# Kernel optimization log

Measured on AMD Instinct MI355X. Metric: run time of the kernel, lower is better.

Reference implementation:

```python
import jax, jax.numpy as jnp
import numpy as np

LN_EPS = 1e-5  # ParlAI LAYER_NORM_EPS
B, S, D, H, E, V = 4, 512, 512, 2048, 8, 32000


def setup_inputs() -> dict:
    key = jax.random.key(0)
    ks = jax.random.split(key, 6)
    x = jax.random.normal(ks[0], (B, S, D), dtype=jnp.float32)
    orig_input = jax.random.randint(ks[1], (B, S), 0, V)          # token ids
    hash_bin_map = jax.random.randint(ks[2], (V,), 0, E, dtype=jnp.int32)
    W1 = jax.random.normal(ks[3], (E, D, H), dtype=jnp.float32) * 0.02
    b1 = jnp.zeros((E, H), dtype=jnp.float32)
    W2 = jax.random.normal(ks[4], (E, H, D), dtype=jnp.float32) * 0.02
    b2 = jnp.zeros((E, D), dtype=jnp.float32)
    gamma = jnp.ones((D,), dtype=jnp.float32)
    beta = jnp.zeros((D,), dtype=jnp.float32)
    return {"x": x, "W1": W1, "b1": b1, "W2": W2, "b2": b2,
            "gamma": gamma, "beta": beta,
            "orig_input": orig_input, "hash_bin_map": hash_bin_map}


def _layernorm(z, gamma, beta):
    mu = jnp.mean(z, axis=-1, keepdims=True)
    var = jnp.var(z, axis=-1, keepdims=True)
    return (z - mu) * jax.lax.rsqrt(var + LN_EPS) * gamma + beta


def reference(x, W1, b1, W2, b2, gamma, beta, orig_input, hash_bin_map):
    # per-token expert assignment via hash of token id
    bins = hash_bin_map[orig_input]                    # [B, S] int
    n_experts = W1.shape[0]
    ffn_out = jnp.zeros_like(x)
    # loop over the small fixed expert set; mask-combine replaces gather/scatter
    for e in range(n_experts):
        h = jax.nn.relu(jnp.einsum('bsd,dh->bsh', x, W1[e]) + b1[e])
        y = jnp.einsum('bsh,hd->bsd', h, W2[e]) + b2[e]
        ffn_out = ffn_out + jnp.where((bins == e)[..., None], y, 0.0)
    # residual + shared LayerNorm (every token belongs to exactly one bin)
    return _layernorm(x + ffn_out, gamma, beta)
```

## Files before the change

kernel.cpp:

```cpp
#include <hip/hip_runtime.h>
#include <hip/hip_bf16.h>
#include <stdint.h>

#define D_DIM 512
#define H_DIM 2048
#define E_NUM 8
#define TM 64
#define CAP 2560
#define MAXRT 6
#define MAXRTB 3

typedef __attribute__((ext_vector_type(8))) short short8;
typedef __attribute__((ext_vector_type(4))) float floatx4;

union Pack4 { short4 u; __hip_bfloat16 h[4]; };

__device__ inline void async16(const void* g, void* s) {
    __builtin_amdgcn_global_load_lds(
        (const __attribute__((address_space(1))) void*)g,
        (__attribute__((address_space(3))) void*)s, 16, 0, 0);
}

__global__ __launch_bounds__(256) void bin_kernel(
    const int* __restrict__ orig, const int* __restrict__ hmap,
    int* __restrict__ gidx, int* __restrict__ meta, int ntok)
{
    __shared__ int cnt[E_NUM];
    __shared__ int cur[E_NUM];
    int tid = threadIdx.x;
    if (tid < E_NUM) cnt[tid] = 0;
    __syncthreads();
    for (int t = tid; t < ntok; t += 256) {
        int b = hmap[orig[t]];
        atomicAdd(&cnt[b], 1);
    }
    __syncthreads();
    if (tid == 0) {
        int off = 0;
        for (int e = 0; e < E_NUM; e++) {
            int ne = cnt[e];
            int nt = (ne + TM - 1) / TM;
            meta[e] = off; meta[8 + e] = ne; meta[16 + e] = nt;
            cur[e] = off;
            off += nt * TM;
        }
        meta[24] = off;
    }
    __syncthreads();
    for (int t = tid; t < ntok; t += 256) {
        int b = hmap[orig[t]];
        int p = atomicAdd(&cur[b], 1);
        gidx[p] = t;
    }
}

__global__ __launch_bounds__(128) void gather_kernel(
    const float* __restrict__ x, const int* __restrict__ gidx,
    const int* __restrict__ meta, __hip_bfloat16* __restrict__ Xg)
{
    int g = blockIdx.x;
    int e = -1, local = 0;
#pragma unroll
    for (int i = 0; i < E_NUM; i++) {
        int p = meta[i], nt = meta[16 + i];
        if (g >= p && g < p + nt * TM) { e = i; local = g - p; }
    }
    if (e < 0) return;
    int tid = threadIdx.x;
    __hip_bfloat16* orow = Xg + (size_t)g * D_DIM + tid * 4;
    if (local < meta[8 + e]) {
        int t = gidx[g];
        float4 v = ((const float4*)(x + (size_t)t * D_DIM))[tid];
        orow[0] = __float2bfloat16(v.x);
        orow[1] = __float2bfloat16(v.y);
        orow[2] = __float2bfloat16(v.z);
        orow[3] = __float2bfloat16(v.w);
    } else {
        orow[0] = __float2bfloat16(0.f);
        orow[1] = __float2bfloat16(0.f);
        orow[2] = __float2bfloat16(0.f);
        orow[3] = __float2bfloat16(0.f);
    }
}

template <int WN, int ASTRIDE, int KTOT, int KS, int RTS, bool RELU>
__global__ __launch_bounds__(256) void moe_gemm_kernel(
    const __hip_bfloat16* __restrict__ A,
    const float* __restrict__ W,
    const float* __restrict__ bias,
    __hip_bfloat16* __restrict__ OutBf,
    float* __restrict__ OutF,
    const int* __restrict__ meta)
{
    constexpr int KLEN = KTOT / KS;
    const int e = blockIdx.z;
    const int n0 = blockIdx.x * 64;
    const int ks = blockIdx.y / RTS;
    const int rts = blockIdx.y % RTS;
    const int kbase = ks * KLEN;

    int nt_e = meta[16 + e];
    if (nt_e > MAXRT) nt_e = MAXRT;
    const int ntb = (nt_e + RTS - 1) / RTS;
    const int rtstart = rts * ntb;
    int myrt = nt_e - rtstart;
    if (myrt > ntb) myrt = ntb;
    if (myrt <= 0) return;
    const int row0 = meta[e] + rtstart * 64;
    const int rows8 = myrt * 64 * 8;

    __shared__ __align__(16) __hip_bfloat16 As[192 * 64];
    __shared__ __align__(16) __hip_bfloat16 Bs[64 * 64];

    const int tid = threadIdx.x;
    const int lane = tid & 63, w = tid >> 6;
    const int quad = lane >> 4, l16 = lane & 15;
    const int wr = w >> 1, wc = w & 1;
    const int kq = tid >> 4;
    const int nb = tid & 15;

    const __hip_bfloat16* Ab = A + (size_t)row0 * ASTRIDE + kbase;
    const float* Wb = W + ((size_t)e * KTOT + kbase) * WN + n0;

    floatx4 acc[MAXRTB][2][2] = {};

    float4 br[4];
#pragma unroll
    for (int r = 0; r < 4; r++)
        br[r] = *(const float4*)(Wb + (size_t)(kq * 4 + r) * WN + nb * 4);

    for (int k0 = 0; k0 < KLEN; k0 += 64) {
        __syncthreads();
        for (int c = tid; c < rows8; c += 256) {
            int row = c >> 3;
            int kk = ((c & 7) * 16) ^ ((row & 7) * 16);
            async16(Ab + (size_t)row * ASTRIDE + k0 + (kk >> 1), (char*)As + c * 16);
        }
#pragma unroll
        for (int j = 0; j < 4; j++) {
            int n = nb * 4 + j;
            Pack4 pk;
#pragma unroll
            for (int r = 0; r < 4; r++)
                pk.h[r] = __float2bfloat16(reinterpret_cast<const float*>(&br[r])[j]);
            *(short4*)((char*)Bs + n * 128 + ((kq * 8) ^ (((n >> 2) & 7) * 16))) = pk.u;
        }
        __syncthreads();
        if (k0 + 64 < KLEN) {
#pragma unroll
            for (int r = 0; r < 4; r++)
                br[r] = *(const float4*)(Wb + (size_t)(k0 + 64 + kq * 4 + r) * WN + nb * 4);
        }
#pragma unroll
        for (int kf = 0; kf < 2; kf++) {
            int kb = kf * 64 + quad * 16;
            short8 b[2];
#pragma unroll
            for (int ni = 0; ni < 2; ni++) {
                int n = wc * 32 + ni * 16 + l16;
                b[ni] = *(const short8*)((char*)Bs + n * 128 + (kb ^ (((n >> 2) & 7) * 16)));
            }
#pragma unroll
            for (int rt = 0; rt < MAXRTB; rt++) {
                if (rt < myrt) {
                    short8 a[2];
#pragma unroll
                    for (int mi = 0; mi < 2; mi++) {
                        int row = rt * 64 + wr * 32 + mi * 16 + l16;
                        a[mi] = *(const short8*)((char*)As + row * 128 + (kb ^ ((row & 7) * 16)));
                    }
#pragma unroll
                    for (int mi = 0; mi < 2; mi++)
#pragma unroll
                        for (int ni = 0; ni < 2; ni++)
                            acc[rt][mi][ni] = __builtin_amdgcn_mfma_f32_16x16x32_bf16(
                                a[mi], b[ni], acc[rt][mi][ni], 0, 0, 0);
                }
            }
        }
    }

#pragma unroll
    for (int rt = 0; rt < MAXRTB; rt++) {
        if (rt >= myrt) break;
#pragma unroll
        for (int ni = 0; ni < 2; ni++) {
            int col = n0 + wc * 32 + ni * 16 + l16;
            float bv = RELU ? bias[e * WN + col] : 0.f;
#pragma unroll
            for (int mi = 0; mi < 2; mi++) {
#pragma unroll
                for (int r = 0; r < 4; r++) {
                    int grow = row0 + rt * 64 + wr * 32 + mi * 16 + quad * 4 + r;
                    float v = acc[rt][mi][ni][r] + bv;
                    if constexpr (RELU) {
                        v = v > 0.f ? v : 0.f;
                        OutBf[(size_t)grow * WN + col] = __float2bfloat16(v);
                    } else {
                        OutF[((size_t)ks * CAP + grow) * WN + col] = v;
                    }
                }
            }
        }
    }
}

__global__ __launch_bounds__(128) void ln_kernel(
    const float* __restrict__ x, const float* __restrict__ Yb,
    const float* __restrict__ b2,
    const float* __restrict__ gamma, const float* __restrict__ beta,
    const int* __restrict__ gidx, const int* __restrict__ meta,
    float* __restrict__ out)
{
    int g = blockIdx.x;
    int e = -1;
#pragma unroll
    for (int i = 0; i < E_NUM; i++) {
        int p = meta[i], ne = meta[8 + i];
        if (g >= p && g - p < ne) e = i;
    }
    if (e < 0) return;
    int t = gidx[g];
    int tid = threadIdx.x;

    float4 xv = ((const float4*)(x + (size_t)t * D_DIM))[tid];
    float4 bb = ((const float4*)(b2 + (size_t)e * D_DIM))[tid];
    float z0 = xv.x + bb.x, z1 = xv.y + bb.y, z2 = xv.z + bb.z, z3 = xv.w + bb.w;
#pragma unroll
    for (int s4 = 0; s4 < 4; s4++) {
        float4 yv = ((const float4*)(Yb + (size_t)(s4 * CAP + g) * D_DIM))[tid];
        z0 += yv.x; z1 += yv.y; z2 += yv.z; z3 += yv.w;
    }

    float s = z0 + z1 + z2 + z3;
    float ss = z0 * z0 + z1 * z1 + z2 * z2 + z3 * z3;
#pragma unroll
    for (int off = 32; off > 0; off >>= 1) {
        s  += __shfl_down(s, off, 64);
        ss += __shfl_down(ss, off, 64);
    }
    __shared__ float red[4];
    int lane = tid & 63, wv = tid >> 6;
    if (lane == 0) { red[wv] = s; red[2 + wv] = ss; }
    __syncthreads();
    float S = red[0] + red[1];
    float SS = red[2] + red[3];
    float mu = S * (1.f / D_DIM);
    float var = SS * (1.f / D_DIM) - mu * mu;
    float inv = rsqrtf(var + 1e-5f);

    float4 gv = ((const float4*)gamma)[tid];
    float4 bv = ((const float4*)beta)[tid];
    float4 o;
    o.x = (z0 - mu) * inv * gv.x + bv.x;
    o.y = (z1 - mu) * inv * gv.y + bv.y;
    o.z = (z2 - mu) * inv * gv.z + bv.z;
    o.w = (z3 - mu) * inv * gv.w + bv.w;
    ((float4*)(out + (size_t)t * D_DIM))[tid] = o;
}

extern "C" void kernel_launch(void* const* d_in, const int* in_sizes, int n_in,
                              void* d_out, int out_size, void* d_ws, size_t ws_size,
                              hipStream_t stream)
{
    const float* x     = (const float*)d_in[0];
    const float* W1    = (const float*)d_in[1];
    const float* b1    = (const float*)d_in[2];
    const float* W2    = (const float*)d_in[3];
    const float* b2    = (const float*)d_in[4];
    const float* gamma = (const float*)d_in[5];
    const float* beta  = (const float*)d_in[6];
    const int* orig    = (const int*)d_in[7];
    const int* hmap    = (const int*)d_in[8];
    float* out = (float*)d_out;
    int ntok = in_sizes[7];

    char* ws = (char*)d_ws;
    float*          Yb  = (float*)(ws);
    __hip_bfloat16* Hb  = (__hip_bfloat16*)(ws + 20971520);
    __hip_bfloat16* Xg  = (__hip_bfloat16*)(ws + 31457280);
    int*            gidx= (int*)(ws + 34078720);
    int*            meta= (int*)(ws + 34088960);

    hipLaunchKernelGGL(bin_kernel, dim3(1), dim3(256), 0, stream,
                       orig, hmap, gidx, meta, ntok);
    hipLaunchKernelGGL(gather_kernel, dim3(CAP), dim3(128), 0, stream,
                       x, gidx, meta, Xg);
    hipLaunchKernelGGL((moe_gemm_kernel<H_DIM, D_DIM, D_DIM, 1, 2, true>),
                       dim3(H_DIM / 64, 2, E_NUM), dim3(256), 0, stream,
                       Xg, W1, b1, Hb, (float*)nullptr, meta);
    hipLaunchKernelGGL((moe_gemm_kernel<D_DIM, H_DIM, H_DIM, 4, 2, false>),
                       dim3(D_DIM / 64, 8, E_NUM), dim3(256), 0, stream,
                       Hb, W2, (const float*)nullptr, (__hip_bfloat16*)nullptr, Yb, meta);
    hipLaunchKernelGGL(ln_kernel, dim3(CAP), dim3(128), 0, stream,
                       x, Yb, b2, gamma, beta, gidx, meta, out);
}
```

Measured before the change: 156.5 us.

## Fuse binning, gather, both expert GEMMs and LayerNorm into one cooperative kernel

Replaces five separate kernel launches with a single cooperative persistent kernel of 512 blocks that runs binning, gather, the two MoE GEMMs and LayerNorm as phases separated by grid-wide syncs. The aim is to remove per-launch overhead and the gaps between kernels. In exchange it adds grid.sync barriers, serialises the binning step on one block while the others wait, and needs two blocks per CU (launch bounds 256,2) for the whole grid to be co-resident, which may limit registers for the GEMM.

```diff
diff --git a/kernel.cpp b/kernel.cpp
--- a/kernel.cpp
+++ b/kernel.cpp
@@ -1,6 +1,9 @@
 #include <hip/hip_runtime.h>
+#include <hip/hip_cooperative_groups.h>
 #include <hip/hip_bf16.h>
 #include <stdint.h>
+
+namespace cg = cooperative_groups;
 
 #define D_DIM 512
 #define H_DIM 2048
@@ -9,6 +12,7 @@
 #define CAP 2560
 #define MAXRT 6
 #define MAXRTB 3
+#define NBLK 512
 
 typedef __attribute__((ext_vector_type(8))) short short8;
 typedef __attribute__((ext_vector_type(4))) float floatx4;
@@ -21,82 +25,18 @@
         (__attribute__((address_space(3))) void*)s, 16, 0, 0);
 }
 
-__global__ __launch_bounds__(256) void bin_kernel(
-    const int* __restrict__ orig, const int* __restrict__ hmap,
-    int* __restrict__ gidx, int* __restrict__ meta, int ntok)
-{
-    __shared__ int cnt[E_NUM];
-    __shared__ int cur[E_NUM];
-    int tid = threadIdx.x;
-    if (tid < E_NUM) cnt[tid] = 0;
-    __syncthreads();
-    for (int t = tid; t < ntok; t += 256) {
-        int b = hmap[orig[t]];
-        atomicAdd(&cnt[b], 1);
-    }
-    __syncthreads();
-    if (tid == 0) {
-        int off = 0;
-        for (int e = 0; e < E_NUM; e++) {
-            int ne = cnt[e];
-            int nt = (ne + TM - 1) / TM;
-            meta[e] = off; meta[8 + e] = ne; meta[16 + e] = nt;
-            cur[e] = off;
-            off += nt * TM;
-        }
-        meta[24] = off;
-    }
-    __syncthreads();
-    for (int t = tid; t < ntok; t += 256) {
-        int b = hmap[orig[t]];
-        int p = atomicAdd(&cur[b], 1);
-        gidx[p] = t;
-    }
-}
-
-__global__ __launch_bounds__(128) void gather_kernel(
-    const float* __restrict__ x, const int* __restrict__ gidx,
-    const int* __restrict__ meta, __hip_bfloat16* __restrict__ Xg)
-{
-    int g = blockIdx.x;
-    int e = -1, local = 0;
-#pragma unroll
-    for (int i = 0; i < E_NUM; i++) {
-        int p = meta[i], nt = meta[16 + i];
-        if (g >= p && g < p + nt * TM) { e = i; local = g - p; }
-    }
-    if (e < 0) return;
-    int tid = threadIdx.x;
-    __hip_bfloat16* orow = Xg + (size_t)g * D_DIM + tid * 4;
-    if (local < meta[8 + e]) {
-        int t = gidx[g];
-        float4 v = ((const float4*)(x + (size_t)t * D_DIM))[tid];
-        orow[0] = __float2bfloat16(v.x);
-        orow[1] = __float2bfloat16(v.y);
-        orow[2] = __float2bfloat16(v.z);
-        orow[3] = __float2bfloat16(v.w);
-    } else {
-        orow[0] = __float2bfloat16(0.f);
-        orow[1] = __float2bfloat16(0.f);
-        orow[2] = __float2bfloat16(0.f);
-        orow[3] = __float2bfloat16(0.f);
-    }
-}
-
 template <int WN, int ASTRIDE, int KTOT, int KS, int RTS, bool RELU>
-__global__ __launch_bounds__(256) void moe_gemm_kernel(
+__device__ void gemm_phase(char* lds,
     const __hip_bfloat16* __restrict__ A,
     const float* __restrict__ W,
     const float* __restrict__ bias,
     __hip_bfloat16* __restrict__ OutBf,
     float* __restrict__ OutF,
-    const int* __restrict__ meta)
+    const int* __restrict__ meta,
+    int e, int nx, int ks, int rts, int tid)
 {
     constexpr int KLEN = KTOT / KS;
-    const int e = blockIdx.z;
-    const int n0 = blockIdx.x * 64;
-    const int ks = blockIdx.y / RTS;
-    const int rts = blockIdx.y % RTS;
+    const int n0 = nx * 64;
     const int kbase = ks * KLEN;
 
     int nt_e = meta[16 + e];
@@ -109,10 +49,9 @@
     const int row0 = meta[e] + rtstart * 64;
     const int rows8 = myrt * 64 * 8;
 
-    __shared__ __align__(16) __hip_bfloat16 As[192 * 64];
-    __shared__ __align__(16) __hip_bfloat16 Bs[64 * 64];
-
-    const int tid = threadIdx.x;
+    __hip_bfloat16* As = (__hip_bfloat16*)lds;
+    __hip_bfloat16* Bs = (__hip_bfloat16*)(lds + 24576);
+
     const int lane = tid & 63, w = tid >> 6;
     const int quad = lane >> 4, l16 = lane & 15;
     const int wr = w >> 1, wc = w & 1;
@@ -205,58 +144,134 @@
     }
 }
 
-__global__ __launch_bounds__(128) void ln_kernel(
-    const float* __restrict__ x, const float* __restrict__ Yb,
-    const float* __restrict__ b2,
+__global__ __launch_bounds__(256, 2) void fused_moe_kernel(
+    const float* __restrict__ x,
+    const float* __restrict__ W1, const float* __restrict__ b1,
+    const float* __restrict__ W2, const float* __restrict__ b2,
     const float* __restrict__ gamma, const float* __restrict__ beta,
-    const int* __restrict__ gidx, const int* __restrict__ meta,
-    float* __restrict__ out)
+    const int* __restrict__ orig, const int* __restrict__ hmap,
+    __hip_bfloat16* __restrict__ Xg, __hip_bfloat16* __restrict__ Hb,
+    float* __restrict__ Yb, int* __restrict__ gidx, int* __restrict__ meta,
+    float* __restrict__ out, int ntok)
 {
-    int g = blockIdx.x;
-    int e = -1;
-#pragma unroll
-    for (int i = 0; i < E_NUM; i++) {
-        int p = meta[i], ne = meta[8 + i];
-        if (g >= p && g - p < ne) e = i;
-    }
-    if (e < 0) return;
-    int t = gidx[g];
-    int tid = threadIdx.x;
-
-    float4 xv = ((const float4*)(x + (size_t)t * D_DIM))[tid];
-    float4 bb = ((const float4*)(b2 + (size_t)e * D_DIM))[tid];
-    float z0 = xv.x + bb.x, z1 = xv.y + bb.y, z2 = xv.z + bb.z, z3 = xv.w + bb.w;
-#pragma unroll
-    for (int s4 = 0; s4 < 4; s4++) {
-        float4 yv = ((const float4*)(Yb + (size_t)(s4 * CAP + g) * D_DIM))[tid];
-        z0 += yv.x; z1 += yv.y; z2 += yv.z; z3 += yv.w;
-    }
-
-    float s = z0 + z1 + z2 + z3;
-    float ss = z0 * z0 + z1 * z1 + z2 * z2 + z3 * z3;
-#pragma unroll
-    for (int off = 32; off > 0; off >>= 1) {
-        s  += __shfl_down(s, off, 64);
-        ss += __shfl_down(ss, off, 64);
-    }
-    __shared__ float red[4];
-    int lane = tid & 63, wv = tid >> 6;
-    if (lane == 0) { red[wv] = s; red[2 + wv] = ss; }
-    __syncthreads();
-    float S = red[0] + red[1];
-    float SS = red[2] + red[3];
-    float mu = S * (1.f / D_DIM);
-    float var = SS * (1.f / D_DIM) - mu * mu;
-    float inv = rsqrtf(var + 1e-5f);
-
-    float4 gv = ((const float4*)gamma)[tid];
-    float4 bv = ((const float4*)beta)[tid];
-    float4 o;
-    o.x = (z0 - mu) * inv * gv.x + bv.x;
-    o.y = (z1 - mu) * inv * gv.y + bv.y;
-    o.z = (z2 - mu) * inv * gv.z + bv.z;
-    o.w = (z3 - mu) * inv * gv.w + bv.w;
-    ((float4*)(out + (size_t)t * D_DIM))[tid] = o;
+    cg::grid_group grid = cg::this_grid();
+    const int bid = blockIdx.x;
+    const int tid = threadIdx.x;
+
+    __shared__ __align__(16) char lds[32768];
+
+    if (bid == 0) {
+        int* cnt = (int*)lds;
+        int* cur = cnt + E_NUM;
+        if (tid < E_NUM) cnt[tid] = 0;
+        __syncthreads();
+        for (int t = tid; t < ntok; t += 256) {
+            int b = hmap[orig[t]];
+            atomicAdd(&cnt[b], 1);
+        }
+        __syncthreads();
+        if (tid == 0) {
+            int off = 0;
+            for (int e = 0; e < E_NUM; e++) {
+                int ne = cnt[e];
+                int nt = (ne + TM - 1) / TM;
+                meta[e] = off; meta[8 + e] = ne; meta[16 + e] = nt;
+                cur[e] = off;
+                off += nt * TM;
+            }
+            meta[24] = off;
+        }
+        __syncthreads();
+        for (int t = tid; t < ntok; t += 256) {
+            int b = hmap[orig[t]];
+            int p = atomicAdd(&cur[b], 1);
+            gidx[p] = t;
+        }
+    }
+    grid.sync();
+
+    for (int g = bid; g < CAP; g += NBLK) {
+        int e = -1, local = 0;
+#pragma unroll
+        for (int i = 0; i < E_NUM; i++) {
+            int p = meta[i], nt = meta[16 + i];
+            if (g >= p && g < p + nt * TM) { e = i; local = g - p; }
+        }
+        if (e < 0) continue;
+        __hip_bfloat16* orow = Xg + (size_t)g * D_DIM + tid * 2;
+        if (local < meta[8 + e]) {
+            int t = gidx[g];
+            float2 v = ((const float2*)(x + (size_t)t * D_DIM))[tid];
+            orow[0] = __float2bfloat16(v.x);
+            orow[1] = __float2bfloat16(v.y);
+        } else {
+            orow[0] = __float2bfloat16(0.f);
+            orow[1] = __float2bfloat16(0.f);
+        }
+    }
+    grid.sync();
+
+    {
+        int nx = bid & 31, rts = (bid >> 5) & 1, e = bid >> 6;
+        gemm_phase<H_DIM, D_DIM, D_DIM, 1, 2, true>(
+            lds, Xg, W1, b1, Hb, (float*)nullptr, meta, e, nx, 0, rts, tid);
+    }
+    grid.sync();
+
+    {
+        int nx = bid & 7, ks = (bid >> 3) & 3, rts = (bid >> 5) & 1, e = bid >> 6;
+        gemm_phase<D_DIM, H_DIM, H_DIM, 4, 2, false>(
+            lds, Hb, W2, (const float*)nullptr, (__hip_bfloat16*)nullptr, Yb, meta,
+            e, nx, ks, rts, tid);
+    }
+    grid.sync();
+
+    {
+        float* red = (float*)lds;
+        for (int g = bid; g < CAP; g += NBLK) {
+            int e = -1;
+#pragma unroll
+            for (int i = 0; i < E_NUM; i++) {
+                int p = meta[i], ne = meta[8 + i];
+                if (g >= p && g - p < ne) e = i;
+            }
+            if (e < 0) continue;
+            int t = gidx[g];
+
+            float2 xv = ((const float2*)(x + (size_t)t * D_DIM))[tid];
+            float2 bb = ((const float2*)(b2 + (size_t)e * D_DIM))[tid];
+            float z0 = xv.x + bb.x, z1 = xv.y + bb.y;
+#pragma unroll
+            for (int s4 = 0; s4 < 4; s4++) {
+                float2 yv = ((const float2*)(Yb + (size_t)(s4 * CAP + g) * D_DIM))[tid];
+                z0 += yv.x; z1 += yv.y;
+            }
+
+            float s = z0 + z1;
+            float ss = z0 * z0 + z1 * z1;
+#pragma unroll
+            for (int off = 32; off > 0; off >>= 1) {
+                s  += __shfl_down(s, off, 64);
+                ss += __shfl_down(ss, off, 64);
+            }
+            int lane = tid & 63, wv = tid >> 6;
+            if (lane == 0) { red[wv] = s; red[4 + wv] = ss; }
+            __syncthreads();
+            float S  = red[0] + red[1] + red[2] + red[3];
+            float SS = red[4] + red[5] + red[6] + red[7];
+            __syncthreads();
+            float mu = S * (1.f / D_DIM);
+            float var = SS * (1.f / D_DIM) - mu * mu;
+            float inv = rsqrtf(var + 1e-5f);
+
+            float2 gv = ((const float2*)gamma)[tid];
+            float2 bv = ((const float2*)beta)[tid];
+            float2 o;
+            o.x = (z0 - mu) * inv * gv.x + bv.x;
+            o.y = (z1 - mu) * inv * gv.y + bv.y;
+            ((float2*)(out + (size_t)t * D_DIM))[tid] = o;
+        }
+    }
 }
 
 extern "C" void kernel_launch(void* const* d_in, const int* in_sizes, int n_in,
@@ -282,16 +297,10 @@
     int*            gidx= (int*)(ws + 34078720);
     int*            meta= (int*)(ws + 34088960);
 
-    hipLaunchKernelGGL(bin_kernel, dim3(1), dim3(256), 0, stream,
-                       orig, hmap, gidx, meta, ntok);
-    hipLaunchKernelGGL(gather_kernel, dim3(CAP), dim3(128), 0, stream,
-                       x, gidx, meta, Xg);
-    hipLaunchKernelGGL((moe_gemm_kernel<H_DIM, D_DIM, D_DIM, 1, 2, true>),
-                       dim3(H_DIM / 64, 2, E_NUM), dim3(256), 0, stream,
-                       Xg, W1, b1, Hb, (float*)nullptr, meta);
-    hipLaunchKernelGGL((moe_gemm_kernel<D_DIM, H_DIM, H_DIM, 4, 2, false>),
-                       dim3(D_DIM / 64, 8, E_NUM), dim3(256), 0, stream,
-                       Hb, W2, (const float*)nullptr, (__hip_bfloat16*)nullptr, Yb, meta);
-    hipLaunchKernelGGL(ln_kernel, dim3(CAP), dim3(128), 0, stream,
-                       x, Yb, b2, gamma, beta, gidx, meta, out);
+    void* args[] = { (void*)&x, (void*)&W1, (void*)&b1, (void*)&W2, (void*)&b2,
+                     (void*)&gamma, (void*)&beta, (void*)&orig, (void*)&hmap,
+                     (void*)&Xg, (void*)&Hb, (void*)&Yb, (void*)&gidx, (void*)&meta,
+                     (void*)&out, (void*)&ntok };
+    hipLaunchCooperativeKernel((const void*)fused_moe_kernel,
+                               dim3(NBLK), dim3(256), args, 0, stream);
 }
```

New measurement: 405.5 us. +159.1%, slower.
